# Performance work log

Measured on AMD Instinct MI355X. Metric: run time of the kernel, lower is better.

The kernel has to match this reference:

```python
import jax, jax.numpy as jnp
import numpy as np

EPS = 1e-12  # torch F.normalize eps


def unfold(x, ksize, pad):
    # torch F.unfold equivalent: [B,C,H,W] -> [B, C*k*k, L], channel-major ordering
    patches = jax.lax.conv_general_dilated_patches(
        x, (ksize, ksize), (1, 1), [(pad, pad), (pad, pad)],
        dimension_numbers=('NCHW', 'OIHW', 'NCHW'))
    B, CKK, Hp, Wp = patches.shape
    return patches.reshape(B, CKK, Hp * Wp)


def fold(patches, C, ksize, H, W, pad):
    # torch F.fold equivalent (stride 1): overlap-add of [B, C*k*k, H*W] -> [B,C,H,W]
    B = patches.shape[0]
    p = patches.reshape(B, C, ksize, ksize, H, W)
    out = jnp.zeros((B, C, H + 2 * pad, W + 2 * pad), patches.dtype)
    for di in range(ksize):
        for dj in range(ksize):
            out = out.at[:, :, di:di + H, dj:dj + W].add(p[:, :, di, dj])
    return out[:, :, pad:pad + H, pad:pad + W]


def setup_inputs() -> dict:
    key = jax.random.key(0)
    ks = jax.random.split(key, 4)
    B, C, H, W = 2, 512, 64, 64
    D, CIN = 256, 512 * 9  # embed: Linear(tdim*8*3*3 -> tdim*4), tdim=64
    return {
        'query': jax.random.normal(ks[0], (B, C, H, W), dtype=jnp.float32),
        'key': jax.random.normal(ks[1], (B, C, H, W), dtype=jnp.float32),
        'value': jax.random.normal(ks[2], (B, C, H, W), dtype=jnp.float32),
        'W_embed': jax.random.normal(ks[3], (D, CIN), dtype=jnp.float32) * 0.02,
        'k': 3,
    }


def reference(query, key, value, W_embed, k):
    B, Cv, H, W = value.shape
    # patch embed: unfold -> linear (no bias)
    q_unf = unfold(query, k, k // 2)                       # [B, C*k*k, L]
    k_unf = unfold(key, k, k // 2)                         # [B, C*k*k, L]
    k_emb = jnp.einsum('bcl,dc->bld', k_unf, W_embed)      # [B, L, D]
    q_emb = jnp.einsum('bcl,dc->bdl', q_unf, W_embed)      # [B, D, L]
    # cosine correlation
    k_n = k_emb / jnp.maximum(jnp.linalg.norm(k_emb, axis=2, keepdims=True), EPS)
    q_n = q_emb / jnp.maximum(jnp.linalg.norm(q_emb, axis=1, keepdims=True), EPS)
    corr = jnp.einsum('bld,bdm->blm', k_n, q_n)            # [B, L_key, L_query]
    corr_value = jnp.max(corr, axis=1)                     # [B, L]
    corr_argmax = jnp.argmax(corr, axis=1)                 # [B, L]
    # swap(V=value, idx=corr_argmax, s=1, k=k)
    s = 1
    temph = s * k + H * s - H - s                          # = k - 1
    tempw = s * k + W * s - W - s
    ph = max(temph // 2 + temph % 2, 1)
    pw = max(tempw // 2 + tempw % 2, 1)
    v_unf = unfold(value, k, ph)                           # [B, Cv*k*k, L] (ph==pw for square)
    t_unf = jnp.take_along_axis(v_unf, corr_argmax[:, None, :], axis=2)
    divisor = fold(jnp.ones_like(t_unf), Cv, k, H, W, ph)
    T = fold(t_unf, Cv, k, H, W, ph) / divisor             # [B, Cv, H, W]
    S = corr_value.reshape(B, 1, H, W)
    return S, T
```

## Files before the change

### kernel.cpp

```cpp
#include <hip/hip_runtime.h>
#include <hip/hip_bf16.h>
#include <stdint.h>
#include <math.h>

#define BB 2
#define CC 512
#define HH 64
#define WW 64
#define LL 4096
#define DD 256
#define CIN 4608
#define NT 144

typedef _Float16 half_t;
typedef __attribute__((ext_vector_type(8))) _Float16 f16x8;
typedef __attribute__((ext_vector_type(4))) _Float16 f16x4;
typedef __attribute__((ext_vector_type(4))) float f32x4;

__global__ __launch_bounds__(256) void splitW2(const float* __restrict__ W,
                                               char* __restrict__ Wst) {
    int i = blockIdx.x * 256 + threadIdx.x;
    if (i >= NT * DD * 4) return;
    int it = i >> 10;
    int r  = i & 1023;
    int d  = r >> 2;
    int fs = r & 3;
    const float* src = W + (size_t)d * CIN + it * 32 + fs * 8;
    f16x8 h8, l8;
#pragma unroll
    for (int j = 0; j < 8; j++) {
        float w = src[j];
        half_t h = (half_t)w;
        h8[j] = h;
        l8[j] = (half_t)(w - (float)h);
    }
    size_t base = (size_t)it * 32768 + d * 128;
    int sw = (d & 7) << 4;
    *(f16x8*)(Wst + base + ((fs * 16) ^ sw)) = h8;
    *(f16x8*)(Wst + base + ((64 + fs * 16) ^ sw)) = l8;
}

__device__ __forceinline__ half_t* ldsAddr(half_t* base, int r, int slot) {
    return base + r * 64 + ((slot ^ (r & 7)) << 3);
}

#define GATE4() do { asm volatile("s_waitcnt vmcnt(4) lgkmcnt(0)" ::: "memory"); \
                     __builtin_amdgcn_s_barrier(); \
                     __builtin_amdgcn_sched_barrier(0); } while (0)
#define GATE0() do { asm volatile("s_waitcnt vmcnt(0) lgkmcnt(0)" ::: "memory"); \
                     __builtin_amdgcn_s_barrier(); \
                     __builtin_amdgcn_sched_barrier(0); } while (0)

__global__ __launch_bounds__(256, 2) void embed_mfma(const float* __restrict__ query,
                                                     const float* __restrict__ key,
                                                     const char* __restrict__ Wst,
                                                     char* __restrict__ qemb,
                                                     char* __restrict__ kemb) {
    __shared__ half_t sW[2][16384];
    __shared__ half_t sB[2][2048];
    __shared__ float red[4][32];
    __shared__ float invn[32];

    int iid = blockIdx.y;
    int b = iid & 1, type = iid >> 1;
    const float* img = (type ? key : query) + (size_t)b * CC * LL;
    int l0 = blockIdx.x * 32;
    int y  = l0 >> 6;
    int x0 = l0 & 63;
    int t = threadIdx.x;
    int w = t >> 6;
    int lane = t & 63;
    int wr = w;
    int fr = lane & 15;
    int fs = lane >> 4;

    int xB = t & 31;
    int kcB = t >> 5;
    int k0 = kcB * 4;
    int cS = k0 / 9;
    int offS = k0 - cS * 9;

    f32x4 acc[4][2];
#pragma unroll
    for (int rg = 0; rg < 4; rg++)
#pragma unroll
        for (int cg = 0; cg < 2; cg++) acc[rg][cg] = (f32x4){0.f, 0.f, 0.f, 0.f};

    float Bv[4];

#define LOADB()                                                          \
    do {                                                                 \
        int cj = cS, oj = offS;                                          \
        _Pragma("unroll")                                                \
        for (int j = 0; j < 4; j++) {                                    \
            int di = oj / 3, dj = oj - di * 3;                           \
            int yy = y + di - 1, xx = x0 + xB + dj - 1;                  \
            int vld = (yy >= 0 && yy < HH && xx >= 0 && xx < WW);        \
            int yc = yy < 0 ? 0 : (yy > HH - 1 ? HH - 1 : yy);           \
            int xc = xx < 0 ? 0 : (xx > WW - 1 ? WW - 1 : xx);           \
            float v = img[(size_t)cj * LL + yc * WW + xc];               \
            Bv[j] = vld ? v : 0.f;                                       \
            oj++; if (oj >= 9) { oj = 0; cj++; }                         \
        }                                                                \
        cS += 3; offS += 5; if (offS >= 9) { offS -= 9; cS++; }          \
    } while (0)

#define WRITEB(buf)                                                      \
    do {                                                                 \
        f16x4 h4, l4;                                                    \
        _Pragma("unroll")                                                \
        for (int j = 0; j < 4; j++) {                                    \
            half_t h = (half_t)Bv[j];                                    \
            h4[j] = h; l4[j] = (half_t)(Bv[j] - (float)h);               \
        }                                                                \
        *(f16x4*)(ldsAddr(buf, xB, kcB >> 1) + ((kcB & 1) << 2)) = h4;   \
        *(f16x4*)(ldsAddr(buf, xB, 4 + (kcB >> 1)) + ((kcB & 1) << 2)) = l4; \
    } while (0)

#define DMAW(swbuf, itv)                                                 \
    do {                                                                 \
        const char* gsrc_ = Wst + (size_t)(itv) * 32768 + (w << 13) + (lane << 4); \
        char* ldst_ = (char*)(swbuf) + (w << 13);                        \
        _Pragma("unroll")                                                \
        for (int c = 0; c < 8; c++)                                      \
            __builtin_amdgcn_global_load_lds(                            \
                (const __attribute__((address_space(1))) void*)(gsrc_ + c * 1024), \
                (__attribute__((address_space(3))) void*)(ldst_ + c * 1024), 16, 0, 0); \
    } while (0)

#define READA(swbuf)                                                     \
    do {                                                                 \
        _Pragma("unroll")                                                \
        for (int rg = 0; rg < 4; rg++) {                                 \
            int dl = wr * 64 + rg * 16 + fr;                             \
            int sw_ = (dl & 7) << 4;                                     \
            const char* rowp = (const char*)(swbuf) + dl * 128;          \
            ah[rg] = *(const f16x8*)(rowp + ((fs * 16) ^ sw_));          \
            al[rg] = *(const f16x8*)(rowp + ((64 + fs * 16) ^ sw_));     \
        }                                                                \
    } while (0)

#define READB(buf)                                                       \
    do {                                                                 \
        _Pragma("unroll")                                                \
        for (int cg = 0; cg < 2; cg++) {                                 \
            int r = cg * 16 + fr;                                        \
            bh[cg] = *(f16x8*)ldsAddr(buf, r, fs);                       \
            bl[cg] = *(f16x8*)ldsAddr(buf, r, fs + 4);                   \
        }                                                                \
    } while (0)

#define DOMFMA()                                                         \
    do {                                                                 \
        _Pragma("unroll")                                                \
        for (int rg = 0; rg < 4; rg++)                                   \
            _Pragma("unroll")                                            \
            for (int cg = 0; cg < 2; cg++)                               \
                acc[rg][cg] = __builtin_amdgcn_mfma_f32_16x16x32_f16(ah[rg], bh[cg], acc[rg][cg], 0, 0, 0); \
        _Pragma("unroll")                                                \
        for (int rg = 0; rg < 4; rg++)                                   \
            _Pragma("unroll")                                            \
            for (int cg = 0; cg < 2; cg++) {                             \
                acc[rg][cg] = __builtin_amdgcn_mfma_f32_16x16x32_f16(ah[rg], bl[cg], acc[rg][cg], 0, 0, 0); \
                acc[rg][cg] = __builtin_amdgcn_mfma_f32_16x16x32_f16(al[rg], bh[cg], acc[rg][cg], 0, 0, 0); \
            }                                                            \
    } while (0)

    f16x8 ah[4], al[4], bh[2], bl[2];

    LOADB();
    DMAW(&sW[0][0], 0);
    __builtin_amdgcn_sched_barrier(0);
    WRITEB(&sB[0][0]);
    __builtin_amdgcn_sched_barrier(0);
    LOADB();

    half_t* swc = &sW[0][0]; half_t* swn = &sW[1][0];
    half_t* sbc = &sB[0][0]; half_t* sbn = &sB[1][0];

    for (int it = 0; it < NT - 1; ++it) {
        GATE4();
        READA(swc);
        READB(sbc);
        WRITEB(sbn);
        __builtin_amdgcn_sched_barrier(0);
        DMAW(swn, it + 1);
        __builtin_amdgcn_sched_barrier(0);
        if (it < NT - 2) LOADB();
        DOMFMA();
        half_t* tp = swc; swc = swn; swn = tp;
        tp = sbc; sbc = sbn; sbn = tp;
    }
    GATE0();
    READA(swc);
    READB(sbc);
    DOMFMA();

    float ss[2] = {0.f, 0.f};
#pragma unroll
    for (int rg = 0; rg < 4; rg++)
#pragma unroll
        for (int cg = 0; cg < 2; cg++)
#pragma unroll
            for (int r = 0; r < 4; r++) ss[cg] += acc[rg][cg][r] * acc[rg][cg][r];
#pragma unroll
    for (int cg = 0; cg < 2; cg++) {
        ss[cg] += __shfl_xor(ss[cg], 16);
        ss[cg] += __shfl_xor(ss[cg], 32);
    }
    if (lane < 16) { red[w][lane] = ss[0]; red[w][16 + lane] = ss[1]; }
    __syncthreads();
    if (t < 32) {
        float s = red[0][t] + red[1][t] + red[2][t] + red[3][t];
        invn[t] = 1.0f / fmaxf(sqrtf(s), 1e-12f);
    }
    __syncthreads();

    char* e = (type == 0) ? qemb : kemb;
#pragma unroll
    for (int cg = 0; cg < 2; cg++) {
        int lloc = cg * 16 + fr;
        float sc = invn[lloc];
        int l = l0 + lloc;
        char* rowp = e + ((size_t)b * LL + l) * 1024;
        int swb = (l & 7) << 4;
#pragma unroll
        for (int rg = 0; rg < 4; rg++) {
            int d0 = wr * 64 + rg * 16 + fs * 4;
            f16x4 h4, l4;
#pragma unroll
            for (int r = 0; r < 4; r++) {
                float v = acc[rg][cg][r] * sc;
                half_t h = (half_t)v;
                h4[r] = h;
                l4[r] = (half_t)(v - (float)h);
            }
            int itb = d0 >> 5;
            int fsc = (d0 >> 3) & 3;
            int sub = (d0 & 7) * 2;
            *(f16x4*)(rowp + itb * 128 + ((fsc * 16) ^ swb) + sub) = h4;
            *(f16x4*)(rowp + itb * 128 + ((64 + fsc * 16) ^ swb) + sub) = l4;
        }
    }
#undef LOADB
#undef WRITEB
#undef DMAW
#undef READA
#undef READB
#undef DOMFMA
}

__global__ void init_packed(unsigned long long* p, int n) {
    int i = blockIdx.x * 256 + threadIdx.x;
    if (i < n) p[i] = 0ull;
}

__global__ __launch_bounds__(256, 2) void corr_max_mfma(const char* __restrict__ kemb,
                                                        const char* __restrict__ qemb,
                                                        unsigned long long* __restrict__ packed) {
    __shared__ char sA[2][16384];
    __shared__ char sBq[2][16384];

    int b  = blockIdx.z;
    int l0 = blockIdx.y * 128;
    int m0 = blockIdx.x * 128;
    int t  = threadIdx.x;
    int w = t >> 6, lane = t & 63;
    int wr = w >> 1, wc = w & 1;
    int fr = lane & 15, fs = lane >> 4;

    const char* Abase = kemb + ((size_t)b * LL + l0) * 1024;
    const char* Bbase = qemb + ((size_t)b * LL + m0) * 1024;

    f32x4 acc[4][4];
#pragma unroll
    for (int i = 0; i < 4; i++)
#pragma unroll
        for (int j = 0; j < 4; j++) acc[i][j] = (f32x4){0.f, 0.f, 0.f, 0.f};

#define DMA2(bufi, itv)                                                   \
    do {                                                                  \
        _Pragma("unroll")                                                 \
        for (int c = 0; c < 4; c++) {                                     \
            int idx = c * 4096 + t * 16;                                  \
            int row = idx >> 7, offb = idx & 127;                         \
            __builtin_amdgcn_global_load_lds(                             \
                (const __attribute__((address_space(1))) void*)(Abase + (size_t)row * 1024 + (itv) * 128 + offb), \
                (__attribute__((address_space(3))) void*)(&sA[bufi][idx]), 16, 0, 0); \
        }                                                                 \
        _Pragma("unroll")                                                 \
        for (int c = 0; c < 4; c++) {                                     \
            int idx = c * 4096 + t * 16;                                  \
            int row = idx >> 7, offb = idx & 127;                         \
            __builtin_amdgcn_global_load_lds(                             \
                (const __attribute__((address_space(1))) void*)(Bbase + (size_t)row * 1024 + (itv) * 128 + offb), \
                (__attribute__((address_space(3))) void*)(&sBq[bufi][idx]), 16, 0, 0); \
        }                                                                 \
    } while (0)

    DMA2(0, 0);

    f16x8 ah[4], al[4], bh[4], bl[4];
    for (int it = 0; it < 8; ++it) {
        asm volatile("s_waitcnt vmcnt(0) lgkmcnt(0)" ::: "memory");
        __builtin_amdgcn_s_barrier();
        __builtin_amdgcn_sched_barrier(0);
        if (it < 7) DMA2((it + 1) & 1, it + 1);
        __builtin_amdgcn_sched_barrier(0);
        const char* sa = sA[it & 1];
        const char* sb = sBq[it & 1];
#pragma unroll
        for (int rg = 0; rg < 4; rg++) {
            int r = wr * 64 + rg * 16 + fr;
            const char* rp = sa + r * 128;
            int sw_ = (r & 7) << 4;
            ah[rg] = *(const f16x8*)(rp + ((fs * 16) ^ sw_));
            al[rg] = *(const f16x8*)(rp + ((64 + fs * 16) ^ sw_));
        }
#pragma unroll
        for (int cg = 0; cg < 4; cg++) {
            int r = wc * 64 + cg * 16 + fr;
            const char* rp = sb + r * 128;
            int sw_ = (r & 7) << 4;
            bh[cg] = *(const f16x8*)(rp + ((fs * 16) ^ sw_));
            bl[cg] = *(const f16x8*)(rp + ((64 + fs * 16) ^ sw_));
        }
#pragma unroll
        for (int rg = 0; rg < 4; rg++)
#pragma unroll
            for (int cg = 0; cg < 4; cg++)
                acc[rg][cg] = __builtin_amdgcn_mfma_f32_16x16x32_f16(ah[rg], bh[cg], acc[rg][cg], 0, 0, 0);
#pragma unroll
        for (int rg = 0; rg < 4; rg++)
#pragma unroll
            for (int cg = 0; cg < 4; cg++) {
                acc[rg][cg] = __builtin_amdgcn_mfma_f32_16x16x32_f16(ah[rg], bl[cg], acc[rg][cg], 0, 0, 0);
                acc[rg][cg] = __builtin_amdgcn_mfma_f32_16x16x32_f16(al[rg], bh[cg], acc[rg][cg], 0, 0, 0);
            }
    }
#undef DMA2

#pragma unroll
    for (int cg = 0; cg < 4; cg++) {
        unsigned long long best = 0ull;
#pragma unroll
        for (int rg = 0; rg < 4; rg++) {
#pragma unroll
            for (int r = 0; r < 4; r++) {
                unsigned u = __float_as_uint(acc[rg][cg][r]);
                u = (u & 0x80000000u) ? ~u : (u | 0x80000000u);
                int l = l0 + wr * 64 + rg * 16 + fs * 4 + r;
                unsigned long long p = ((unsigned long long)u << 32) | (unsigned)(4095 - l);
                best = (p > best) ? p : best;
            }
        }
        unsigned long long o;
        o = __shfl_xor(best, 16); best = (o > best) ? o : best;
        o = __shfl_xor(best, 32); best = (o > best) ? o : best;
        if (lane < 16)
            atomicMax(&packed[(size_t)b * LL + m0 + wc * 64 + cg * 16 + lane], best);
    }
}

__global__ void decode_packed(const unsigned long long* __restrict__ packed,
                              float* __restrict__ S_out, int* __restrict__ arg) {
    int i = blockIdx.x * 256 + threadIdx.x;
    if (i < BB * LL) {
        unsigned long long p = packed[i];
        unsigned u = (unsigned)(p >> 32);
        unsigned bits = (u & 0x80000000u) ? (u & 0x7FFFFFFFu) : ~u;
        S_out[i] = __uint_as_float(bits);
        arg[i] = 4095 - (int)(unsigned)(p & 0xFFFFFFFFull);
    }
}

__global__ __launch_bounds__(256) void transpose_mat(const float* __restrict__ src,
                                                     float* __restrict__ dst,
                                                     int R, int Cc) {
    __shared__ float tile[32][33];
    size_t boff = (size_t)blockIdx.z * R * Cc;
    int bx = blockIdx.x;
    int by = blockIdx.y;
    int tx = threadIdx.x & 31;
    int ty = threadIdx.x >> 5;
    const float* s = src + boff;
    float* d = dst + boff;
#pragma unroll
    for (int i = 0; i < 4; i++) {
        int r = by * 32 + ty + i * 8;
        int c = bx * 32 + tx;
        tile[ty + i * 8][tx] = s[(size_t)r * Cc + c];
    }
    __syncthreads();
#pragma unroll
    for (int i = 0; i < 4; i++) {
        int c = bx * 32 + ty + i * 8;
        int r = by * 32 + tx;
        d[(size_t)c * R + r] = tile[tx][ty + i * 8];
    }
}

__global__ __launch_bounds__(256) void gather_fold(const float* __restrict__ value_t,
                                                   const int* __restrict__ arg,
                                                   float* __restrict__ T_t) {
    int b = blockIdx.y;
    int pix = blockIdx.x;
    int y = pix >> 6, x = pix & 63;
    int t = threadIdx.x;
    float2 acc = make_float2(0.f, 0.f);
    int cnty = (y == 0 || y == HH - 1) ? 2 : 3;
    int cntx = (x == 0 || x == WW - 1) ? 2 : 3;
    const int* ab = arg + b * LL;
    const float* vb = value_t + (size_t)b * LL * CC;
#pragma unroll
    for (int di = 0; di < 3; di++) {
        int my = y + 1 - di;
        if (my < 0 || my >= HH) continue;
#pragma unroll
        for (int dj = 0; dj < 3; dj++) {
            int mx = x + 1 - dj;
            if (mx < 0 || mx >= WW) continue;
            int a = ab[my * WW + mx];
            int ay = a >> 6, ax = a & 63;
            int vy = ay + di - 1, vx = ax + dj - 1;
            if (vy < 0 || vy >= HH || vx < 0 || vx >= WW) continue;
            float2 v = *(const float2*)&vb[((size_t)(vy * WW + vx)) * CC + t * 2];
            acc.x += v.x; acc.y += v.y;
        }
    }
    float inv = 1.0f / (float)(cnty * cntx);
    acc.x *= inv; acc.y *= inv;
    *(float2*)&T_t[((size_t)b * LL + pix) * CC + t * 2] = acc;
}

extern "C" void kernel_launch(void* const* d_in, const int* in_sizes, int n_in,
                              void* d_out, int out_size, void* d_ws, size_t ws_size,
                              hipStream_t stream) {
    const float* query = (const float*)d_in[0];
    const float* key   = (const float*)d_in[1];
    const float* value = (const float*)d_in[2];
    const float* Wemb  = (const float*)d_in[3];

    float* out   = (float*)d_out;
    float* S_out = out;
    float* T_out = out + BB * LL;

    char* ws = (char*)d_ws;
    size_t off = 0;
    char* Wst  = ws + off; off += (size_t)NT * 32768;
    char* qemb = ws + off; off += (size_t)BB * LL * 1024;
    char* kemb = ws + off; off += (size_t)BB * LL * 1024;
    float* val_t = (float*)(ws + off); off += (size_t)BB * LL * CC * 4;
    unsigned long long* packed = (unsigned long long*)(ws + off); off += (size_t)BB * LL * 8;
    int* arg = (int*)(ws + off); off += (size_t)BB * LL * 4;
    float* T_t = (float*)ws;

    splitW2       <<<dim3(576), 256, 0, stream>>>(Wemb, Wst);
    embed_mfma    <<<dim3(128, 4), 256, 0, stream>>>(query, key, Wst, qemb, kemb);
    init_packed   <<<dim3(32), 256, 0, stream>>>(packed, BB * LL);
    corr_max_mfma <<<dim3(32, 32, 2), 256, 0, stream>>>(kemb, qemb, packed);
    decode_packed <<<dim3(32), 256, 0, stream>>>(packed, S_out, arg);
    transpose_mat <<<dim3(128, 16, 2), 256, 0, stream>>>(value, val_t, CC, LL);
    gather_fold   <<<dim3(4096, 2), 256, 0, stream>>>(val_t, arg, T_t);
    transpose_mat <<<dim3(16, 128, 2), 256, 0, stream>>>(T_t, T_out, LL, CC);
}
```

Baseline: 255.3 us.

## Widen embed tile to full image row with 512-thread blocks

The embed GEMM block now covers a whole 64-pixel row with 8 waves arranged 4x2, so each W tile loaded into LDS serves twice as many output pixels. Global W traffic for the embed stage is halved, and the im2col gather now uses precomputed row and column offsets with clamping in place of divisions. The grid shrinks to 256 blocks of 512 threads with one block per CU, which lowers occupancy and may leave part of the 256-CU device idle or underfed.

```diff
diff --git a/kernel.cpp b/kernel.cpp
--- a/kernel.cpp
+++ b/kernel.cpp
@@ -51,34 +51,40 @@
                      __builtin_amdgcn_s_barrier(); \
                      __builtin_amdgcn_sched_barrier(0); } while (0)
 
-__global__ __launch_bounds__(256, 2) void embed_mfma(const float* __restrict__ query,
+__global__ __launch_bounds__(512, 1) void embed_mfma(const float* __restrict__ query,
                                                      const float* __restrict__ key,
                                                      const char* __restrict__ Wst,
                                                      char* __restrict__ qemb,
                                                      char* __restrict__ kemb) {
     __shared__ half_t sW[2][16384];
-    __shared__ half_t sB[2][2048];
-    __shared__ float red[4][32];
-    __shared__ float invn[32];
+    __shared__ half_t sB[2][4096];
+    __shared__ float red[4][64];
+    __shared__ float invn[64];
 
     int iid = blockIdx.y;
     int b = iid & 1, type = iid >> 1;
-    const float* img = (type ? key : query) + (size_t)b * CC * LL;
-    int l0 = blockIdx.x * 32;
-    int y  = l0 >> 6;
-    int x0 = l0 & 63;
+    const char* imgB = (const char*)((type ? key : query) + (size_t)b * CC * LL);
+    int y  = blockIdx.x;
+    int l0 = y * 64;
     int t = threadIdx.x;
     int w = t >> 6;
     int lane = t & 63;
-    int wr = w;
+    int wr = w >> 1;
+    int wc = w & 1;
     int fr = lane & 15;
     int fs = lane >> 4;
 
-    int xB = t & 31;
-    int kcB = t >> 5;
-    int k0 = kcB * 4;
-    int cS = k0 / 9;
-    int offS = k0 - cS * 9;
+    int xB = t & 63;
+    int kcB = __builtin_amdgcn_readfirstlane(t >> 6);
+    int cS = (kcB * 4) / 9;
+    int offS = (kcB * 4) % 9;
+
+    int row0 = (y > 0 ? y - 1 : 0) * 256;  int vy0 = (y > 0);
+    int row1 = y * 256;
+    int row2 = (y < 63 ? y + 1 : 63) * 256; int vy2 = (y < 63);
+    int X0 = (xB > 0 ? xB - 1 : 0) * 4;    int vx0 = (xB > 0);
+    int X1 = xB * 4;
+    int X2 = (xB < 63 ? xB + 1 : 63) * 4;  int vx2 = (xB < 63);
 
     f32x4 acc[4][2];
 #pragma unroll
@@ -93,13 +99,14 @@
         int cj = cS, oj = offS;                                          \
         _Pragma("unroll")                                                \
         for (int j = 0; j < 4; j++) {                                    \
-            int di = oj / 3, dj = oj - di * 3;                           \
-            int yy = y + di - 1, xx = x0 + xB + dj - 1;                  \
-            int vld = (yy >= 0 && yy < HH && xx >= 0 && xx < WW);        \
-            int yc = yy < 0 ? 0 : (yy > HH - 1 ? HH - 1 : yy);           \
-            int xc = xx < 0 ? 0 : (xx > WW - 1 ? WW - 1 : xx);           \
-            float v = img[(size_t)cj * LL + yc * WW + xc];               \
-            Bv[j] = vld ? v : 0.f;                                       \
+            int di = (oj >= 6) ? 2 : (oj >= 3) ? 1 : 0;                  \
+            int dj = oj - di * 3;                                        \
+            int rowb = (di == 0) ? row0 : (di == 1) ? row1 : row2;       \
+            int vy   = (di == 0) ? vy0 : (di == 1) ? 1 : vy2;            \
+            int xoff = (dj == 0) ? X0 : (dj == 1) ? X1 : X2;             \
+            int vx   = (dj == 0) ? vx0 : (dj == 1) ? 1 : vx2;            \
+            float v = *(const float*)(imgB + (((size_t)cj) << 14) + rowb + xoff); \
+            Bv[j] = (vy & vx) ? v : 0.f;                                 \
             oj++; if (oj >= 9) { oj = 0; cj++; }                         \
         }                                                                \
         cS += 3; offS += 5; if (offS >= 9) { offS -= 9; cS++; }          \
@@ -119,13 +126,13 @@
 
 #define DMAW(swbuf, itv)                                                 \
     do {                                                                 \
-        const char* gsrc_ = Wst + (size_t)(itv) * 32768 + (w << 13) + (lane << 4); \
-        char* ldst_ = (char*)(swbuf) + (w << 13);                        \
-        _Pragma("unroll")                                                \
-        for (int c = 0; c < 8; c++)                                      \
+        const char* gsrc_ = Wst + (size_t)(itv) * 32768 + t * 16;        \
+        char* ldst_ = (char*)(swbuf) + t * 16;                           \
+        _Pragma("unroll")                                                \
+        for (int c = 0; c < 4; c++)                                      \
             __builtin_amdgcn_global_load_lds(                            \
-                (const __attribute__((address_space(1))) void*)(gsrc_ + c * 1024), \
-                (__attribute__((address_space(3))) void*)(ldst_ + c * 1024), 16, 0, 0); \
+                (const __attribute__((address_space(1))) void*)(gsrc_ + c * 8192), \
+                (__attribute__((address_space(3))) void*)(ldst_ + c * 8192), 16, 0, 0); \
     } while (0)
 
 #define READA(swbuf)                                                     \
@@ -144,7 +151,7 @@
     do {                                                                 \
         _Pragma("unroll")                                                \
         for (int cg = 0; cg < 2; cg++) {                                 \
-            int r = cg * 16 + fr;                                        \
+            int r = wc * 32 + cg * 16 + fr;                              \
             bh[cg] = *(f16x8*)ldsAddr(buf, r, fs);                       \
             bl[cg] = *(f16x8*)ldsAddr(buf, r, fs + 4);                   \
         }                                                                \
@@ -208,9 +215,12 @@
         ss[cg] += __shfl_xor(ss[cg], 16);
         ss[cg] += __shfl_xor(ss[cg], 32);
     }
-    if (lane < 16) { red[w][lane] = ss[0]; red[w][16 + lane] = ss[1]; }
+    if (lane < 16) {
+        red[wr][wc * 32 + lane] = ss[0];
+        red[wr][wc * 32 + 16 + lane] = ss[1];
+    }
     __syncthreads();
-    if (t < 32) {
+    if (t < 64) {
         float s = red[0][t] + red[1][t] + red[2][t] + red[3][t];
         invn[t] = 1.0f / fmaxf(sqrtf(s), 1e-12f);
     }
@@ -219,7 +229,7 @@
     char* e = (type == 0) ? qemb : kemb;
 #pragma unroll
     for (int cg = 0; cg < 2; cg++) {
-        int lloc = cg * 16 + fr;
+        int lloc = wc * 32 + cg * 16 + fr;
         float sc = invn[lloc];
         int l = l0 + lloc;
         char* rowp = e + ((size_t)b * LL + l) * 1024;
@@ -456,7 +466,7 @@
     float* T_t = (float*)ws;
 
     splitW2       <<<dim3(576), 256, 0, stream>>>(Wemb, Wst);
-    embed_mfma    <<<dim3(128, 4), 256, 0, stream>>>(query, key, Wst, qemb, kemb);
+    embed_mfma    <<<dim3(64, 4), 512, 0, stream>>>(query, key, Wst, qemb, kemb);
     init_packed   <<<dim3(32), 256, 0, stream>>>(packed, BB * LL);
     corr_max_mfma <<<dim3(32, 32, 2), 256, 0, stream>>>(kemb, qemb, packed);
     decode_packed <<<dim3(32), 256, 0, stream>>>(packed, S_out, arg);
```

New measurement: 258.3 us. No clear change (+1.2%).
